# Kernel optimization log

Hardware: AMD Instinct MI355X
Metric: run time of the kernel (lower is better)

Reference implementation:

```python
import jax, jax.numpy as jnp
import numpy as np


def setup_inputs() -> dict:
    key = jax.random.key(0)
    k1, k2, k3, k4 = jax.random.split(key, 4)
    n, L, h = 512, 257, 256
    l = L - 1
    hidden, n_labels = 256, 50
    feat = jax.random.normal(k1, (n, L, h), dtype=jnp.float32)
    heads = jax.random.randint(k2, (n, l), 0, L, dtype=jnp.int64)
    masks = jnp.ones((n, l), dtype=jnp.float32)
    # torch nn.Linear layout: (out_features, in_features); xavier-normal-ish scale
    W1 = jax.random.normal(k3, (hidden, 2 * h), dtype=jnp.float32) * (2.0 / (hidden + 2 * h)) ** 0.5
    b1 = jnp.zeros((hidden,), dtype=jnp.float32)
    W2 = jax.random.normal(k4, (n_labels, hidden), dtype=jnp.float32) * (2.0 / (n_labels + hidden)) ** 0.5
    b2 = jnp.zeros((n_labels,), dtype=jnp.float32)
    return {"feat": feat, "heads": heads, "masks": masks,
            "W1": W1, "b1": b1, "W2": W2, "b2": b2}


def reference(feat, heads, masks, W1, b1, W2, b2):
    # feat: (n, L, h); heads: (n, l) with l = L-1, values in [0, L)
    dependent_f = feat[:, 1:, :]                                   # (n, l, h)
    # head_f[b, i] = feat[b, heads[b, i]]  (the gather)
    head_f = jnp.take_along_axis(feat, heads[:, :, None], axis=1)   # (n, l, h)
    cat_f = jnp.concatenate((dependent_f, head_f), axis=2)          # (n, l, 2h)
    hid = jax.nn.relu(jnp.einsum('nlh,oh->nlo', cat_f, W1) + b1)    # (n, l, hidden); dropout is identity at eval
    label_f = jnp.einsum('nlo,ko->nlk', hid, W2) + b2               # (n, l, n_labels)
    return label_f
```

## Files before the change

kernel.cpp:

```cpp
#include <hip/hip_runtime.h>
#include <hip/hip_bf16.h>
#include <stdint.h>

#define AS1 __attribute__((address_space(1)))
#define AS3 __attribute__((address_space(3)))

typedef __bf16 bf16x8 __attribute__((ext_vector_type(8)));
typedef __bf16 bf16x4 __attribute__((ext_vector_type(4)));
typedef float  floatx4 __attribute__((ext_vector_type(4)));

static constexpr int NB   = 512;
static constexpr int LL   = 257;
static constexpr int HH   = 256;
static constexpr int M    = NB * (LL - 1);
static constexpr int K1   = 2 * HH;
static constexpr int NLAB = 50;
static constexpr int CAT_RS = 40;

__device__ __forceinline__ void async16(const void* gptr, void* ldsptr) {
  __builtin_amdgcn_global_load_lds((const AS1 void*)gptr, (AS3 void*)ldsptr, 16, 0, 0);
}

__global__ void prep_w(const float* __restrict__ W1, const float* __restrict__ W2,
                       __bf16* __restrict__ w1b, __bf16* __restrict__ w2b) {
  int idx = blockIdx.x * 256 + threadIdx.x;
  if (idx < 16384) {
    const float4* s = (const float4*)(W1 + (size_t)idx * 8);
    float4 a = s[0], b = s[1];
    bf16x8 v;
    v[0]=(__bf16)a.x; v[1]=(__bf16)a.y; v[2]=(__bf16)a.z; v[3]=(__bf16)a.w;
    v[4]=(__bf16)b.x; v[5]=(__bf16)b.y; v[6]=(__bf16)b.z; v[7]=(__bf16)b.w;
    *(bf16x8*)(w1b + (size_t)idx * 8) = v;
  } else {
    int j = idx - 16384;
    int row = j >> 5;
    int col = (j & 31) * 8;
    float4 a = {0.f,0.f,0.f,0.f}, b = {0.f,0.f,0.f,0.f};
    if (row < NLAB) {
      const float4* s = (const float4*)(W2 + (size_t)row * 256 + col);
      a = s[0]; b = s[1];
    }
    bf16x8 v;
    v[0]=(__bf16)a.x; v[1]=(__bf16)a.y; v[2]=(__bf16)a.z; v[3]=(__bf16)a.w;
    v[4]=(__bf16)b.x; v[5]=(__bf16)b.y; v[6]=(__bf16)b.z; v[7]=(__bf16)b.w;
    *(bf16x8*)(w2b + (size_t)j * 8) = v;
  }
}

__global__ __launch_bounds__(256, 4)
void fused_kernel(const float* __restrict__ feat, const int* __restrict__ heads,
                  const __bf16* __restrict__ w1b, const float* __restrict__ b1,
                  const __bf16* __restrict__ w2b, const float* __restrict__ b2,
                  float* __restrict__ out) {
  __shared__ __align__(16) char smem[32768];
  __bf16* catS = (__bf16*)smem;
  __bf16* W1s  = (__bf16*)(smem + 5120);
  __bf16* hidS = (__bf16*)smem;

  const int t    = threadIdx.x;
  const int w    = t >> 6;
  const int lane = t & 63;
  const int lr   = lane & 15;
  const int q    = lane >> 4;
  const int mBase = blockIdx.x * 64;

  const int r  = t >> 2;
  const int cc = t & 3;
  const int m  = mBase + r;
  const int seq = m >> 8;
  const float* depP  = feat + ((size_t)(seq * LL + (m & 255) + 1)) * HH + cc * 8;
  const float* headP = feat + ((size_t)(seq * LL + heads[m])) * HH + cc * 8;
  __bf16* catW = catS + r * CAT_RS + cc * 8;

  const int gw = ((t & 3) ^ ((t >> 3) & 3)) * 8;
  const __bf16* w1base = w1b + (size_t)(t >> 2) * K1 + gw;

  floatx4 acc[4][4];
  #pragma unroll
  for (int i = 0; i < 4; ++i)
    #pragma unroll
    for (int j = 0; j < 4; ++j)
      acc[i][j] = (floatx4){0.f, 0.f, 0.f, 0.f};

  const int posw = (q ^ ((lr >> 1) & 3)) * 8;

  for (int kt = 0; kt < 16; ++kt) {
    __syncthreads();
    {
      const float* src = (kt < 8) ? depP : headP;
      const int kk = (kt & 7) * 32;
      float4 g0 = *(const float4*)(src + kk);
      float4 g1 = *(const float4*)(src + kk + 4);
      const __bf16* ws = w1base + kt * 32;
      async16(ws,                      W1s + t * 8);
      async16(ws + (size_t)64  * K1,   W1s + (t + 256) * 8);
      async16(ws + (size_t)128 * K1,   W1s + (t + 512) * 8);
      async16(ws + (size_t)192 * K1,   W1s + (t + 768) * 8);
      bf16x8 cv;
      cv[0]=(__bf16)g0.x; cv[1]=(__bf16)g0.y; cv[2]=(__bf16)g0.z; cv[3]=(__bf16)g0.w;
      cv[4]=(__bf16)g1.x; cv[5]=(__bf16)g1.y; cv[6]=(__bf16)g1.z; cv[7]=(__bf16)g1.w;
      *(bf16x8*)catW = cv;
    }
    __syncthreads();

    bf16x8 af[4], bb[4];
    #pragma unroll
    for (int oi = 0; oi < 4; ++oi) {
      const int o = w * 64 + oi * 16 + lr;
      af[oi] = *(const bf16x8*)(W1s + o * 32 + posw);
    }
    #pragma unroll
    for (int mi = 0; mi < 4; ++mi)
      bb[mi] = *(const bf16x8*)(catS + (mi * 16 + lr) * CAT_RS + q * 8);
    #pragma unroll
    for (int oi = 0; oi < 4; ++oi)
      #pragma unroll
      for (int mi = 0; mi < 4; ++mi)
        acc[oi][mi] = __builtin_amdgcn_mfma_f32_16x16x32_bf16(af[oi], bb[mi], acc[oi][mi], 0, 0, 0);
  }

  __syncthreads();

  bf16x8 w2f[8];
  #pragma unroll
  for (int kt2 = 0; kt2 < 8; ++kt2)
    w2f[kt2] = *(const bf16x8*)(w2b + (size_t)(w * 16 + lr) * 256 + kt2 * 32 + q * 8);

  float4 biasv[4];
  #pragma unroll
  for (int oi = 0; oi < 4; ++oi)
    biasv[oi] = *(const float4*)(b1 + w * 64 + oi * 16 + q * 4);

  #pragma unroll
  for (int mi = 0; mi < 4; ++mi) {
    const int mr = mi * 16 + lr;
    const int s  = lr & 7;
    #pragma unroll
    for (int oi = 0; oi < 4; ++oi) {
      const int cj = w * 8 + oi * 2 + (q >> 1);
      bf16x4 hv;
      const float* bp = (const float*)&biasv[oi];
      #pragma unroll
      for (int rr = 0; rr < 4; ++rr) {
        float v = acc[oi][mi][rr] + bp[rr];
        v = v > 0.f ? v : 0.f;
        hv[rr] = (__bf16)v;
      }
      *(bf16x4*)(hidS + mr * 256 + ((cj ^ s) << 3) + (q & 1) * 4) = hv;
    }
  }
  __syncthreads();

  floatx4 acc2[4];
  #pragma unroll
  for (int i = 0; i < 4; ++i) acc2[i] = (floatx4){0.f, 0.f, 0.f, 0.f};

  #pragma unroll
  for (int kt2 = 0; kt2 < 8; ++kt2) {
    #pragma unroll
    for (int mi = 0; mi < 4; ++mi) {
      const int gc = kt2 * 4 + q;
      bf16x8 a2 = *(const bf16x8*)(hidS + (mi * 16 + lr) * 256 + ((gc ^ (lr & 7)) << 3));
      acc2[mi] = __builtin_amdgcn_mfma_f32_16x16x32_bf16(a2, w2f[kt2], acc2[mi], 0, 0, 0);
    }
  }

  const int col = w * 16 + lr;
  if (col < NLAB) {
    const float bias = b2[col];
    #pragma unroll
    for (int mi = 0; mi < 4; ++mi) {
      const int rowBase = mBase + mi * 16 + q * 4;
      #pragma unroll
      for (int rr = 0; rr < 4; ++rr)
        out[(size_t)(rowBase + rr) * NLAB + col] = acc2[mi][rr] + bias;
    }
  }
}

extern "C" void kernel_launch(void* const* d_in, const int* in_sizes, int n_in,
                              void* d_out, int out_size, void* d_ws, size_t ws_size,
                              hipStream_t stream) {
  const float* feat  = (const float*)d_in[0];
  const int*   heads = (const int*)d_in[1];
  const float* W1 = (const float*)d_in[3];
  const float* b1 = (const float*)d_in[4];
  const float* W2 = (const float*)d_in[5];
  const float* b2 = (const float*)d_in[6];
  float* out = (float*)d_out;

  __bf16* w1b = (__bf16*)d_ws;
  __bf16* w2b = w1b + 256 * 512;

  prep_w<<<72, 256, 0, stream>>>(W1, W2, w1b, w2b);
  fused_kernel<<<M / 64, 256, 0, stream>>>(feat, heads, w1b, b1, w2b, b2, out);
}
```

Baseline: 261.1 us.

## Double-buffer LDS K-tiles with prefetched feat loads and coalesced output store

The GEMM1 k-loop is now software-pipelined. Feat rows are prefetched two tiles ahead into registers with inline-asm loads, and W1 tiles are double-buffered in LDS, so each iteration needs one barrier guarded by manual vmcnt waits instead of two __syncthreads. W1 is pre-laid out in tile-major order so each async LDS load is contiguous, and the cat tile uses an XOR swizzle instead of padding. The output is staged through LDS and written with coalesced float4 stores. The cost is more LDS per block (40 KB), which may limit occupancy, plus fragile hand-counted waitcnt values.

```diff
diff --git a/kernel.cpp b/kernel.cpp
--- a/kernel.cpp
+++ b/kernel.cpp
@@ -15,22 +15,37 @@
 static constexpr int M    = NB * (LL - 1);
 static constexpr int K1   = 2 * HH;
 static constexpr int NLAB = 50;
-static constexpr int CAT_RS = 40;
 
 __device__ __forceinline__ void async16(const void* gptr, void* ldsptr) {
   __builtin_amdgcn_global_load_lds((const AS1 void*)gptr, (AS3 void*)ldsptr, 16, 0, 0);
 }
 
+__device__ __forceinline__ floatx4 gload4(const float* p) {
+  floatx4 v;
+  asm volatile("global_load_dwordx4 %0, %1, off" : "=v"(v) : "v"(p) : "memory");
+  return v;
+}
+
+__device__ __forceinline__ bf16x8 cvt8(floatx4 a, floatx4 b) {
+  bf16x8 v;
+  v[0]=(__bf16)a[0]; v[1]=(__bf16)a[1]; v[2]=(__bf16)a[2]; v[3]=(__bf16)a[3];
+  v[4]=(__bf16)b[0]; v[5]=(__bf16)b[1]; v[6]=(__bf16)b[2]; v[7]=(__bf16)b[3];
+  return v;
+}
+
 __global__ void prep_w(const float* __restrict__ W1, const float* __restrict__ W2,
-                       __bf16* __restrict__ w1b, __bf16* __restrict__ w2b) {
+                       __bf16* __restrict__ w1bt, __bf16* __restrict__ w2b) {
   int idx = blockIdx.x * 256 + threadIdx.x;
   if (idx < 16384) {
-    const float4* s = (const float4*)(W1 + (size_t)idx * 8);
+    int o  = idx >> 6;
+    int kc = idx & 63;
+    const float4* s = (const float4*)(W1 + (size_t)o * K1 + kc * 8);
     float4 a = s[0], b = s[1];
     bf16x8 v;
     v[0]=(__bf16)a.x; v[1]=(__bf16)a.y; v[2]=(__bf16)a.z; v[3]=(__bf16)a.w;
     v[4]=(__bf16)b.x; v[5]=(__bf16)b.y; v[6]=(__bf16)b.z; v[7]=(__bf16)b.w;
-    *(bf16x8*)(w1b + (size_t)idx * 8) = v;
+    int kt = kc >> 2, c = kc & 3;
+    *(bf16x8*)(w1bt + ((size_t)((kt * 4 + c) * 256 + o)) * 8) = v;
   } else {
     int j = idx - 16384;
     int row = j >> 5;
@@ -49,13 +64,15 @@
 
 __global__ __launch_bounds__(256, 4)
 void fused_kernel(const float* __restrict__ feat, const int* __restrict__ heads,
-                  const __bf16* __restrict__ w1b, const float* __restrict__ b1,
+                  const __bf16* __restrict__ w1bt, const float* __restrict__ b1,
                   const __bf16* __restrict__ w2b, const float* __restrict__ b2,
                   float* __restrict__ out) {
-  __shared__ __align__(16) char smem[32768];
-  __bf16* catS = (__bf16*)smem;
-  __bf16* W1s  = (__bf16*)(smem + 5120);
-  __bf16* hidS = (__bf16*)smem;
+  __shared__ __align__(16) char smem[40960];
+  __bf16* catS0 = (__bf16*)smem;
+  __bf16* W1s0  = (__bf16*)(smem + 4096);
+  __bf16* catS1 = (__bf16*)(smem + 20480);
+  __bf16* W1s1  = (__bf16*)(smem + 24576);
+  __bf16* hidS  = (__bf16*)smem;
 
   const int t    = threadIdx.x;
   const int w    = t >> 6;
@@ -68,12 +85,10 @@
   const int cc = t & 3;
   const int m  = mBase + r;
   const int seq = m >> 8;
+  const int hidx = heads[m];
   const float* depP  = feat + ((size_t)(seq * LL + (m & 255) + 1)) * HH + cc * 8;
-  const float* headP = feat + ((size_t)(seq * LL + heads[m])) * HH + cc * 8;
-  __bf16* catW = catS + r * CAT_RS + cc * 8;
-
-  const int gw = ((t & 3) ^ ((t >> 3) & 3)) * 8;
-  const __bf16* w1base = w1b + (size_t)(t >> 2) * K1 + gw;
+  const float* headP = feat + ((size_t)(seq * LL + hidx)) * HH + cc * 8;
+  const int catWoff = (r * 4 + (cc ^ ((r >> 1) & 3))) * 8;
 
   floatx4 acc[4][4];
   #pragma unroll
@@ -82,41 +97,73 @@
     for (int j = 0; j < 4; ++j)
       acc[i][j] = (floatx4){0.f, 0.f, 0.f, 0.f};
 
-  const int posw = (q ^ ((lr >> 1) & 3)) * 8;
-
+  const int pcs = q ^ ((lr >> 1) & 3);
+
+  floatx4 gA0, gB0, gA1, gB1;
+
+  gA0 = gload4(depP);
+  gB0 = gload4(depP + 4);
+  {
+    const __bf16* ws = w1bt + t * 8;
+    async16(ws,        W1s0 + t * 8);
+    async16(ws + 2048, W1s0 + (t + 256) * 8);
+    async16(ws + 4096, W1s0 + (t + 512) * 8);
+    async16(ws + 6144, W1s0 + (t + 768) * 8);
+  }
+  gA1 = gload4(depP + 32);
+  gB1 = gload4(depP + 36);
+  asm volatile("s_waitcnt vmcnt(6)" : "+v"(gA0), "+v"(gB0));
+  *(bf16x8*)(catS0 + catWoff) = cvt8(gA0, gB0);
+  asm volatile("s_waitcnt vmcnt(2) lgkmcnt(0)" ::: "memory");
+  __builtin_amdgcn_s_barrier();
+
+  #pragma unroll
   for (int kt = 0; kt < 16; ++kt) {
-    __syncthreads();
-    {
-      const float* src = (kt < 8) ? depP : headP;
-      const int kk = (kt & 7) * 32;
-      float4 g0 = *(const float4*)(src + kk);
-      float4 g1 = *(const float4*)(src + kk + 4);
-      const __bf16* ws = w1base + kt * 32;
-      async16(ws,                      W1s + t * 8);
-      async16(ws + (size_t)64  * K1,   W1s + (t + 256) * 8);
-      async16(ws + (size_t)128 * K1,   W1s + (t + 512) * 8);
-      async16(ws + (size_t)192 * K1,   W1s + (t + 768) * 8);
-      bf16x8 cv;
-      cv[0]=(__bf16)g0.x; cv[1]=(__bf16)g0.y; cv[2]=(__bf16)g0.z; cv[3]=(__bf16)g0.w;
-      cv[4]=(__bf16)g1.x; cv[5]=(__bf16)g1.y; cv[6]=(__bf16)g1.z; cv[7]=(__bf16)g1.w;
-      *(bf16x8*)catW = cv;
-    }
-    __syncthreads();
+    __bf16* catC = (kt & 1) ? catS1 : catS0;
+    __bf16* W1C  = (kt & 1) ? W1s1  : W1s0;
+    __bf16* catN = (kt & 1) ? catS0 : catS1;
+    __bf16* W1N  = (kt & 1) ? W1s0  : W1s1;
+
+    if (kt < 15) {
+      const __bf16* ws = w1bt + (size_t)(kt + 1) * 8192 + t * 8;
+      async16(ws,        W1N + t * 8);
+      async16(ws + 2048, W1N + (t + 256) * 8);
+      async16(ws + 4096, W1N + (t + 512) * 8);
+      async16(ws + 6144, W1N + (t + 768) * 8);
+    }
+    if (kt < 14) {
+      const float* s = (((kt + 2) < 8) ? depP : headP) + ((kt + 2) & 7) * 32;
+      if (kt & 1) { gA1 = gload4(s); gB1 = gload4(s + 4); }
+      else        { gA0 = gload4(s); gB0 = gload4(s + 4); }
+    }
 
     bf16x8 af[4], bb[4];
     #pragma unroll
-    for (int oi = 0; oi < 4; ++oi) {
-      const int o = w * 64 + oi * 16 + lr;
-      af[oi] = *(const bf16x8*)(W1s + o * 32 + posw);
-    }
+    for (int oi = 0; oi < 4; ++oi)
+      af[oi] = *(const bf16x8*)(W1C + (q * 256 + w * 64 + oi * 16 + lr) * 8);
     #pragma unroll
     for (int mi = 0; mi < 4; ++mi)
-      bb[mi] = *(const bf16x8*)(catS + (mi * 16 + lr) * CAT_RS + q * 8);
+      bb[mi] = *(const bf16x8*)(catC + (mi * 64 + lr * 4 + pcs) * 8);
     #pragma unroll
     for (int oi = 0; oi < 4; ++oi)
       #pragma unroll
       for (int mi = 0; mi < 4; ++mi)
         acc[oi][mi] = __builtin_amdgcn_mfma_f32_16x16x32_bf16(af[oi], bb[mi], acc[oi][mi], 0, 0, 0);
+
+    if (kt < 15) {
+      if (kt & 1) {
+        if (kt < 14) asm volatile("s_waitcnt vmcnt(6)" : "+v"(gA0), "+v"(gB0));
+        else         asm volatile("s_waitcnt vmcnt(4)" : "+v"(gA0), "+v"(gB0));
+        *(bf16x8*)(catN + catWoff) = cvt8(gA0, gB0);
+      } else {
+        if (kt < 14) asm volatile("s_waitcnt vmcnt(6)" : "+v"(gA1), "+v"(gB1));
+        else         asm volatile("s_waitcnt vmcnt(4)" : "+v"(gA1), "+v"(gB1));
+        *(bf16x8*)(catN + catWoff) = cvt8(gA1, gB1);
+      }
+      if (kt < 14) asm volatile("s_waitcnt vmcnt(2) lgkmcnt(0)" ::: "memory");
+      else         asm volatile("s_waitcnt vmcnt(0) lgkmcnt(0)" ::: "memory");
+      __builtin_amdgcn_s_barrier();
+    }
   }
 
   __syncthreads();
@@ -164,18 +211,26 @@
       acc2[mi] = __builtin_amdgcn_mfma_f32_16x16x32_bf16(a2, w2f[kt2], acc2[mi], 0, 0, 0);
     }
   }
-
+  __syncthreads();
+
+  float* outT = (float*)smem;
   const int col = w * 16 + lr;
   if (col < NLAB) {
     const float bias = b2[col];
     #pragma unroll
     for (int mi = 0; mi < 4; ++mi) {
-      const int rowBase = mBase + mi * 16 + q * 4;
+      const int rowB = mi * 16 + q * 4;
       #pragma unroll
       for (int rr = 0; rr < 4; ++rr)
-        out[(size_t)(rowBase + rr) * NLAB + col] = acc2[mi][rr] + bias;
-    }
-  }
+        outT[(rowB + rr) * NLAB + col] = acc2[mi][rr] + bias;
+    }
+  }
+  __syncthreads();
+
+  float* odst = out + (size_t)mBase * NLAB;
+  #pragma unroll
+  for (int i = t; i < 800; i += 256)
+    *(float4*)(odst + i * 4) = *(const float4*)(outT + i * 4);
 }
 
 extern "C" void kernel_launch(void* const* d_in, const int* in_sizes, int n_in,
@@ -189,9 +244,9 @@
   const float* b2 = (const float*)d_in[6];
   float* out = (float*)d_out;
 
-  __bf16* w1b = (__bf16*)d_ws;
-  __bf16* w2b = w1b + 256 * 512;
-
-  prep_w<<<72, 256, 0, stream>>>(W1, W2, w1b, w2b);
-  fused_kernel<<<M / 64, 256, 0, stream>>>(feat, heads, w1b, b1, w2b, b2, out);
-}
+  __bf16* w1bt = (__bf16*)d_ws;
+  __bf16* w2b  = w1bt + 256 * 512;
+
+  prep_w<<<72, 256, 0, stream>>>(W1, W2, w1bt, w2b);
+  fused_kernel<<<M / 64, 256, 0, stream>>>(feat, heads, w1bt, b1, w2b, b2, out);
+}
```

Measured after the change: 239.8 us. 1.09x faster.

## Software-pipeline W1 and feature loads into registers with 128-row tiles

Applied to the files above, without the earlier changes.

Doubles the row tile to 128 per block and replaces per-step LDS staging of W1 with direct register loads from a transposed bf16 W1 layout, prefetched one step ahead. Feature rows are loaded three steps ahead into registers and written into a double-buffered LDS cat tile, which needs only one barrier per k-step instead of two. Output is staged through LDS for coalesced float4 stores. The aim is to hide global latency and halve W1 traffic per row, at the cost of more registers and lower occupancy (launch bounds go from 4 to 2 blocks per unit).

```diff
diff --git a/kernel.cpp b/kernel.cpp
--- a/kernel.cpp
+++ b/kernel.cpp
@@ -9,28 +9,42 @@
 typedef __bf16 bf16x4 __attribute__((ext_vector_type(4)));
 typedef float  floatx4 __attribute__((ext_vector_type(4)));
 
-static constexpr int NB   = 512;
 static constexpr int LL   = 257;
 static constexpr int HH   = 256;
-static constexpr int M    = NB * (LL - 1);
-static constexpr int K1   = 2 * HH;
+static constexpr int M    = 131072;
+static constexpr int K1   = 512;
 static constexpr int NLAB = 50;
-static constexpr int CAT_RS = 40;
-
-__device__ __forceinline__ void async16(const void* gptr, void* ldsptr) {
-  __builtin_amdgcn_global_load_lds((const AS1 void*)gptr, (AS3 void*)ldsptr, 16, 0, 0);
+
+#define MFMA_ACC(ACC, A, B) \
+  asm("v_mfma_f32_16x16x32_bf16 %0, %1, %2, %0" : "+a"(ACC) : "v"(A), "v"(B))
+
+template<int IMM>
+__device__ __forceinline__ floatx4 gload4i(const float* p) {
+  floatx4 v;
+  asm volatile("global_load_dwordx4 %0, %1, off offset:%2"
+               : "=v"(v) : "v"(p), "i"(IMM) : "memory");
+  return v;
+}
+
+__device__ __forceinline__ bf16x8 cvt8(floatx4 a, floatx4 b) {
+  bf16x8 v;
+  v[0]=(__bf16)a[0]; v[1]=(__bf16)a[1]; v[2]=(__bf16)a[2]; v[3]=(__bf16)a[3];
+  v[4]=(__bf16)b[0]; v[5]=(__bf16)b[1]; v[6]=(__bf16)b[2]; v[7]=(__bf16)b[3];
+  return v;
 }
 
 __global__ void prep_w(const float* __restrict__ W1, const float* __restrict__ W2,
-                       __bf16* __restrict__ w1b, __bf16* __restrict__ w2b) {
+                       __bf16* __restrict__ w1bt, __bf16* __restrict__ w2b) {
   int idx = blockIdx.x * 256 + threadIdx.x;
   if (idx < 16384) {
-    const float4* s = (const float4*)(W1 + (size_t)idx * 8);
+    int o  = idx >> 6;
+    int kc = idx & 63;
+    const float4* s = (const float4*)(W1 + (size_t)o * K1 + kc * 8);
     float4 a = s[0], b = s[1];
     bf16x8 v;
     v[0]=(__bf16)a.x; v[1]=(__bf16)a.y; v[2]=(__bf16)a.z; v[3]=(__bf16)a.w;
     v[4]=(__bf16)b.x; v[5]=(__bf16)b.y; v[6]=(__bf16)b.z; v[7]=(__bf16)b.w;
-    *(bf16x8*)(w1b + (size_t)idx * 8) = v;
+    *(bf16x8*)(w1bt + ((size_t)(kc * 256 + o)) * 8) = v;
   } else {
     int j = idx - 16384;
     int row = j >> 5;
@@ -47,14 +61,75 @@
   }
 }
 
-__global__ __launch_bounds__(256, 4)
+template<int KT>
+__device__ __forceinline__ void kstep(
+    floatx4 (&catP)[3][4], floatx4 (&afc)[4], floatx4 (&afn)[4],
+    floatx4 (&acc)[4][8],
+    const float* depP0, const float* depP1,
+    const float* headP0, const float* headP1,
+    const __bf16* afBase, const __bf16* catS, int bbOff, __bf16* catW0) {
+
+  if constexpr (KT < 15) {
+    const __bf16* afp = afBase + (KT + 1) * 8192;
+    afn[0] = gload4i<0>((const float*)afp);
+    afn[1] = gload4i<256>((const float*)afp);
+    afn[2] = gload4i<512>((const float*)afp);
+    afn[3] = gload4i<768>((const float*)afp);
+  }
+  if constexpr (KT <= 12) {
+    constexpr int CT  = KT + 3;
+    constexpr int OFF = (CT & 7) * 128;
+    const float* p0 = (CT < 8) ? depP0 : headP0;
+    const float* p1 = (CT < 8) ? depP1 : headP1;
+    catP[KT % 3][0] = gload4i<OFF>(p0);
+    catP[KT % 3][1] = gload4i<OFF + 16>(p0);
+    catP[KT % 3][2] = gload4i<OFF>(p1);
+    catP[KT % 3][3] = gload4i<OFF + 16>(p1);
+  }
+
+  floatx4 (&cs)[4] = catP[(KT + 1) % 3];
+  if constexpr (KT <= 12)
+    asm volatile("s_waitcnt vmcnt(12)" : "+v"(afc[0]),"+v"(afc[1]),"+v"(afc[2]),"+v"(afc[3]),
+                                         "+v"(cs[0]),"+v"(cs[1]),"+v"(cs[2]),"+v"(cs[3]));
+  else if constexpr (KT == 13)
+    asm volatile("s_waitcnt vmcnt(8)"  : "+v"(afc[0]),"+v"(afc[1]),"+v"(afc[2]),"+v"(afc[3]),
+                                         "+v"(cs[0]),"+v"(cs[1]),"+v"(cs[2]),"+v"(cs[3]));
+  else if constexpr (KT == 14)
+    asm volatile("s_waitcnt vmcnt(4)"  : "+v"(afc[0]),"+v"(afc[1]),"+v"(afc[2]),"+v"(afc[3]),
+                                         "+v"(cs[0]),"+v"(cs[1]),"+v"(cs[2]),"+v"(cs[3]));
+  else
+    asm volatile("s_waitcnt vmcnt(0)"  : "+v"(afc[0]),"+v"(afc[1]),"+v"(afc[2]),"+v"(afc[3]),
+                                         "+v"(cs[0]),"+v"(cs[1]),"+v"(cs[2]),"+v"(cs[3]));
+
+  const __bf16* crd = catS + (KT & 1) * 4096 + bbOff;
+  bf16x8 bb[8];
+  #pragma unroll
+  for (int mi = 0; mi < 8; ++mi)
+    bb[mi] = *(const bf16x8*)(crd + mi * 512);
+  #pragma unroll
+  for (int oi = 0; oi < 4; ++oi) {
+    bf16x8 a = __builtin_bit_cast(bf16x8, afc[oi]);
+    #pragma unroll
+    for (int mi = 0; mi < 8; ++mi)
+      MFMA_ACC(acc[oi][mi], a, bb[mi]);
+  }
+
+  if constexpr (KT < 15) {
+    __bf16* cw = catW0 + ((KT + 1) & 1) * 4096;
+    *(bf16x8*)cw          = cvt8(cs[0], cs[1]);
+    *(bf16x8*)(cw + 2048) = cvt8(cs[2], cs[3]);
+    asm volatile("s_waitcnt lgkmcnt(0)" ::: "memory");
+    __builtin_amdgcn_s_barrier();
+  }
+}
+
+__global__ __launch_bounds__(256, 2)
 void fused_kernel(const float* __restrict__ feat, const int* __restrict__ heads,
-                  const __bf16* __restrict__ w1b, const float* __restrict__ b1,
+                  const __bf16* __restrict__ w1bt, const float* __restrict__ b1,
                   const __bf16* __restrict__ w2b, const float* __restrict__ b2,
                   float* __restrict__ out) {
-  __shared__ __align__(16) char smem[32768];
+  __shared__ __align__(16) char smem[65536];
   __bf16* catS = (__bf16*)smem;
-  __bf16* W1s  = (__bf16*)(smem + 5120);
   __bf16* hidS = (__bf16*)smem;
 
   const int t    = threadIdx.x;
@@ -62,62 +137,66 @@
   const int lane = t & 63;
   const int lr   = lane & 15;
   const int q    = lane >> 4;
-  const int mBase = blockIdx.x * 64;
-
-  const int r  = t >> 2;
+  const int mBase = blockIdx.x * 128;
+
+  const int r0 = t >> 2;
   const int cc = t & 3;
-  const int m  = mBase + r;
-  const int seq = m >> 8;
-  const float* depP  = feat + ((size_t)(seq * LL + (m & 255) + 1)) * HH + cc * 8;
-  const float* headP = feat + ((size_t)(seq * LL + heads[m])) * HH + cc * 8;
-  __bf16* catW = catS + r * CAT_RS + cc * 8;
-
-  const int gw = ((t & 3) ^ ((t >> 3) & 3)) * 8;
-  const __bf16* w1base = w1b + (size_t)(t >> 2) * K1 + gw;
-
-  floatx4 acc[4][4];
+  const int m0 = mBase + r0;
+  const int m1 = m0 + 64;
+  const int seq = m0 >> 8;
+  const float* depP0  = feat + ((size_t)(seq * LL + (m0 & 255) + 1)) * HH + cc * 8;
+  const float* depP1  = feat + ((size_t)(seq * LL + (m1 & 255) + 1)) * HH + cc * 8;
+  const float* headP0 = feat + ((size_t)(seq * LL + heads[m0])) * HH + cc * 8;
+  const float* headP1 = feat + ((size_t)(seq * LL + heads[m1])) * HH + cc * 8;
+  asm volatile("" : "+v"(headP0), "+v"(headP1));
+
+  const int pos0 = r0 * 4 + (cc ^ ((r0 >> 1) & 3));
+  __bf16* catW0 = catS + pos0 * 8;
+  const int bbOff = lr * 32 + (q ^ ((lr >> 1) & 3)) * 8;
+  const __bf16* afBase = w1bt + ((size_t)(q * 256 + w * 64 + lr)) * 8;
+
+  floatx4 acc[4][8];
   #pragma unroll
   for (int i = 0; i < 4; ++i)
     #pragma unroll
-    for (int j = 0; j < 4; ++j)
+    for (int j = 0; j < 8; ++j)
       acc[i][j] = (floatx4){0.f, 0.f, 0.f, 0.f};
 
-  const int posw = (q ^ ((lr >> 1) & 3)) * 8;
-
-  for (int kt = 0; kt < 16; ++kt) {
-    __syncthreads();
-    {
-      const float* src = (kt < 8) ? depP : headP;
-      const int kk = (kt & 7) * 32;
-      float4 g0 = *(const float4*)(src + kk);
-      float4 g1 = *(const float4*)(src + kk + 4);
-      const __bf16* ws = w1base + kt * 32;
-      async16(ws,                      W1s + t * 8);
-      async16(ws + (size_t)64  * K1,   W1s + (t + 256) * 8);
-      async16(ws + (size_t)128 * K1,   W1s + (t + 512) * 8);
-      async16(ws + (size_t)192 * K1,   W1s + (t + 768) * 8);
-      bf16x8 cv;
-      cv[0]=(__bf16)g0.x; cv[1]=(__bf16)g0.y; cv[2]=(__bf16)g0.z; cv[3]=(__bf16)g0.w;
-      cv[4]=(__bf16)g1.x; cv[5]=(__bf16)g1.y; cv[6]=(__bf16)g1.z; cv[7]=(__bf16)g1.w;
-      *(bf16x8*)catW = cv;
-    }
-    __syncthreads();
-
-    bf16x8 af[4], bb[4];
-    #pragma unroll
-    for (int oi = 0; oi < 4; ++oi) {
-      const int o = w * 64 + oi * 16 + lr;
-      af[oi] = *(const bf16x8*)(W1s + o * 32 + posw);
-    }
-    #pragma unroll
-    for (int mi = 0; mi < 4; ++mi)
-      bb[mi] = *(const bf16x8*)(catS + (mi * 16 + lr) * CAT_RS + q * 8);
-    #pragma unroll
-    for (int oi = 0; oi < 4; ++oi)
-      #pragma unroll
-      for (int mi = 0; mi < 4; ++mi)
-        acc[oi][mi] = __builtin_amdgcn_mfma_f32_16x16x32_bf16(af[oi], bb[mi], acc[oi][mi], 0, 0, 0);
-  }
+  floatx4 catP[3][4];
+  floatx4 afA[4], afB[4];
+
+  catP[0][0] = gload4i<0>(depP0);    catP[0][1] = gload4i<16>(depP0);
+  catP[0][2] = gload4i<0>(depP1);    catP[0][3] = gload4i<16>(depP1);
+  catP[1][0] = gload4i<128>(depP0);  catP[1][1] = gload4i<144>(depP0);
+  catP[1][2] = gload4i<128>(depP1);  catP[1][3] = gload4i<144>(depP1);
+  afA[0] = gload4i<0>((const float*)afBase);
+  afA[1] = gload4i<256>((const float*)afBase);
+  afA[2] = gload4i<512>((const float*)afBase);
+  afA[3] = gload4i<768>((const float*)afBase);
+  catP[2][0] = gload4i<256>(depP0);  catP[2][1] = gload4i<272>(depP0);
+  catP[2][2] = gload4i<256>(depP1);  catP[2][3] = gload4i<272>(depP1);
+  asm volatile("s_waitcnt vmcnt(12)" : "+v"(catP[0][0]),"+v"(catP[0][1]),"+v"(catP[0][2]),"+v"(catP[0][3]));
+  *(bf16x8*)catW0          = cvt8(catP[0][0], catP[0][1]);
+  *(bf16x8*)(catW0 + 2048) = cvt8(catP[0][2], catP[0][3]);
+  asm volatile("s_waitcnt lgkmcnt(0)" ::: "memory");
+  __builtin_amdgcn_s_barrier();
+
+  kstep< 0>(catP, afA, afB, acc, depP0, depP1, headP0, headP1, afBase, catS, bbOff, catW0);
+  kstep< 1>(catP, afB, afA, acc, depP0, depP1, headP0, headP1, afBase, catS, bbOff, catW0);
+  kstep< 2>(catP, afA, afB, acc, depP0, depP1, headP0, headP1, afBase, catS, bbOff, catW0);
+  kstep< 3>(catP, afB, afA, acc, depP0, depP1, headP0, headP1, afBase, catS, bbOff, catW0);
+  kstep< 4>(catP, afA, afB, acc, depP0, depP1, headP0, headP1, afBase, catS, bbOff, catW0);
+  kstep< 5>(catP, afB, afA, acc, depP0, depP1, headP0, headP1, afBase, catS, bbOff, catW0);
+  kstep< 6>(catP, afA, afB, acc, depP0, depP1, headP0, headP1, afBase, catS, bbOff, catW0);
+  kstep< 7>(catP, afB, afA, acc, depP0, depP1, headP0, headP1, afBase, catS, bbOff, catW0);
+  kstep< 8>(catP, afA, afB, acc, depP0, depP1, headP0, headP1, afBase, catS, bbOff, catW0);
+  kstep< 9>(catP, afB, afA, acc, depP0, depP1, headP0, headP1, afBase, catS, bbOff, catW0);
+  kstep<10>(catP, afA, afB, acc, depP0, depP1, headP0, headP1, afBase, catS, bbOff, catW0);
+  kstep<11>(catP, afB, afA, acc, depP0, depP1, headP0, headP1, afBase, catS, bbOff, catW0);
+  kstep<12>(catP, afA, afB, acc, depP0, depP1, headP0, headP1, afBase, catS, bbOff, catW0);
+  kstep<13>(catP, afB, afA, acc, depP0, depP1, headP0, headP1, afBase, catS, bbOff, catW0);
+  kstep<14>(catP, afA, afB, acc, depP0, depP1, headP0, headP1, afBase, catS, bbOff, catW0);
+  kstep<15>(catP, afB, afA, acc, depP0, depP1, headP0, headP1, afBase, catS, bbOff, catW0);
 
   __syncthreads();
 
@@ -132,7 +211,7 @@
     biasv[oi] = *(const float4*)(b1 + w * 64 + oi * 16 + q * 4);
 
   #pragma unroll
-  for (int mi = 0; mi < 4; ++mi) {
+  for (int mi = 0; mi < 8; ++mi) {
     const int mr = mi * 16 + lr;
     const int s  = lr & 7;
     #pragma unroll
@@ -151,31 +230,39 @@
   }
   __syncthreads();
 
-  floatx4 acc2[4];
-  #pragma unroll
-  for (int i = 0; i < 4; ++i) acc2[i] = (floatx4){0.f, 0.f, 0.f, 0.f};
+  floatx4 acc2[8];
+  #pragma unroll
+  for (int i = 0; i < 8; ++i) acc2[i] = (floatx4){0.f, 0.f, 0.f, 0.f};
 
   #pragma unroll
   for (int kt2 = 0; kt2 < 8; ++kt2) {
-    #pragma unroll
-    for (int mi = 0; mi < 4; ++mi) {
-      const int gc = kt2 * 4 + q;
+    const int gc = kt2 * 4 + q;
+    #pragma unroll
+    for (int mi = 0; mi < 8; ++mi) {
       bf16x8 a2 = *(const bf16x8*)(hidS + (mi * 16 + lr) * 256 + ((gc ^ (lr & 7)) << 3));
       acc2[mi] = __builtin_amdgcn_mfma_f32_16x16x32_bf16(a2, w2f[kt2], acc2[mi], 0, 0, 0);
     }
   }
-
+  __syncthreads();
+
+  float* outT = (float*)smem;
   const int col = w * 16 + lr;
   if (col < NLAB) {
     const float bias = b2[col];
     #pragma unroll
-    for (int mi = 0; mi < 4; ++mi) {
-      const int rowBase = mBase + mi * 16 + q * 4;
+    for (int mi = 0; mi < 8; ++mi) {
+      const int rowB = mi * 16 + q * 4;
       #pragma unroll
       for (int rr = 0; rr < 4; ++rr)
-        out[(size_t)(rowBase + rr) * NLAB + col] = acc2[mi][rr] + bias;
-    }
-  }
+        outT[(rowB + rr) * NLAB + col] = acc2[mi][rr] + bias;
+    }
+  }
+  __syncthreads();
+
+  float* odst = out + (size_t)mBase * NLAB;
+  #pragma unroll
+  for (int i = t; i < 1600; i += 256)
+    *(float4*)(odst + i * 4) = *(const float4*)(outT + i * 4);
 }
 
 extern "C" void kernel_launch(void* const* d_in, const int* in_sizes, int n_in,
@@ -189,9 +276,9 @@
   const float* b2 = (const float*)d_in[6];
   float* out = (float*)d_out;
 
-  __bf16* w1b = (__bf16*)d_ws;
-  __bf16* w2b = w1b + 256 * 512;
-
-  prep_w<<<72, 256, 0, stream>>>(W1, W2, w1b, w2b);
-  fused_kernel<<<M / 64, 256, 0, stream>>>(feat, heads, w1b, b1, w2b, b2, out);
-}
+  __bf16* w1bt = (__bf16*)d_ws;
+  __bf16* w2b  = w1bt + 256 * 512;
+
+  prep_w<<<72, 256, 0, stream>>>(W1, W2, w1bt, w2b);
+  fused_kernel<<<M / 128, 256, 0, stream>>>(feat, heads, w1bt, b1, w2b, b2, out);
+}
```

After: 231.7 us. -11.2%, faster.
